# Performance work log

Measured on AMD Instinct MI355X. Metric: run time of the kernel, lower is better.

Reference implementation:

```python
import jax, jax.numpy as jnp
import numpy as np

PI = float(np.pi)


def _layernorm(x, g, b, eps=1e-5):
    mu = jnp.mean(x, axis=-1, keepdims=True)
    var = jnp.var(x, axis=-1, keepdims=True)
    return (x - mu) * jax.lax.rsqrt(var + eps) * g + b


def setup_inputs() -> dict:
    key = jax.random.key(0)
    B, L, D, P = 4, 2048, 256, 32
    ks = jax.random.split(key, 16)

    def lin_w(k, fi, fo):
        return (jax.random.normal(k, (fi, fo), dtype=jnp.float32) / np.sqrt(fi)).astype(jnp.float32)

    inp = {
        'x': jax.random.normal(ks[0], (B, L, D), dtype=jnp.float32),
        'pos_phases': jax.random.normal(ks[1], (L, P), dtype=jnp.float32) * PI,
        'w_mem1v': lin_w(ks[2], D, P), 'b_mem1v': jnp.zeros((P,), jnp.float32),
        'w_mem1o': lin_w(ks[3], P, D), 'b_mem1o': jnp.zeros((D,), jnp.float32),
        'w_off': lin_w(ks[4], D + P, P), 'b_off': jnp.zeros((P,), jnp.float32),
        'w_key': lin_w(ks[5], D, P), 'b_key': jnp.zeros((P,), jnp.float32),
        'w_val': lin_w(ks[6], D, D), 'b_val': jnp.zeros((D,), jnp.float32),
        'w_sk1': lin_w(ks[7], 2 * D, D), 'b_sk1': jnp.zeros((D,), jnp.float32),
        'w_sk2': lin_w(ks[8], D, P), 'b_sk2': jnp.zeros((P,), jnp.float32),
        'w_gate': lin_w(ks[9], D, 1), 'b_gate': jnp.zeros((1,), jnp.float32),
        'ln_g': jnp.ones((D,), jnp.float32), 'ln_b': jnp.zeros((D,), jnp.float32),
        'w_out': lin_w(ks[10], D, D), 'b_out': jnp.zeros((D,), jnp.float32),
    }
    return inp


def reference(x, pos_phases, w_mem1v, b_mem1v, w_mem1o, b_mem1o, w_off, b_off,
              w_key, b_key, w_val, b_val, w_sk1, b_sk1, w_sk2, b_sk2,
              w_gate, b_gate, ln_g, ln_b, w_out, b_out):
    B, L, D = x.shape
    P = pos_phases.shape[-1]

    pos_cos = jnp.cos(pos_phases)  # [L,P]
    pos_sin = jnp.sin(pos_phases)

    # Memory 1: flat [B,L,P] phasor cumulative memory
    v1 = x @ w_mem1v + b_mem1v                       # [B,L,P]
    mem1_cos = jnp.cumsum(pos_cos[None] * v1, axis=1)
    mem1_sin = jnp.cumsum(pos_sin[None] * v1, axis=1)

    offset_input = jnp.concatenate([x, jnp.broadcast_to(pos_phases[None], (B, L, P))], axis=-1)
    offset = jnp.tanh(offset_input @ w_off + b_off) * PI
    oc, os = jnp.cos(offset), jnp.sin(offset)
    query_cos = pos_cos[None] * oc - pos_sin[None] * os
    query_sin = pos_sin[None] * oc + pos_cos[None] * os
    pos_ret = (mem1_cos * query_cos + mem1_sin * query_sin) / np.sqrt(P)
    pos_out = pos_ret @ w_mem1o + b_mem1o            # [B,L,D]

    # Memory 2: full [B,L,P,D] phasor KV cumulative memory
    key_phases = jnp.tanh(x @ w_key + b_key) * PI    # [B,L,P]
    key_cos, key_sin = jnp.cos(key_phases), jnp.sin(key_phases)
    values = x @ w_val + b_val                       # [B,L,D]
    store_gate = jax.nn.sigmoid(x @ w_gate + b_gate) # [B,L,1]

    positions = jnp.arange(1, L + 1, dtype=x.dtype)[None, :, None]
    context_avg = jnp.cumsum(x, axis=1) / positions
    h = jax.nn.gelu(jnp.concatenate([x, context_avg], axis=-1) @ w_sk1 + b_sk1, approximate=False)
    storage_phases = jnp.tanh(h @ w_sk2 + b_sk2) * PI  # [B,L,P]

    gated_v = values * store_gate                    # [B,L,D]
    kv_mem_cos = jnp.cumsum(jnp.cos(storage_phases)[..., None] * gated_v[:, :, None, :], axis=1)  # [B,L,P,D]
    kv_mem_sin = jnp.cumsum(jnp.sin(storage_phases)[..., None] * gated_v[:, :, None, :], axis=1)

    gate_cumsum = jnp.clip(jnp.cumsum(store_gate, axis=1), 1.0, None)  # [B,L,1]
    kv_retrieved = jnp.einsum('blpd,blp->bld', kv_mem_cos, key_cos) + \
                   jnp.einsum('blpd,blp->bld', kv_mem_sin, key_sin)
    kv_retrieved = kv_retrieved / (jnp.sqrt(gate_cumsum) * np.sqrt(P))

    combined = pos_out + kv_retrieved
    return x + _layernorm(combined, ln_g, ln_b) @ w_out + b_out
```

## Files before the change

kernel.cpp:

```cpp
#include <hip/hip_runtime.h>
#include <hip/hip_bf16.h>

constexpr int B_ = 4;
constexpr int L_ = 2048;
constexpr int D_ = 256;
constexpr int P_ = 32;
constexpr int CL = 32;
constexpr int NC = L_ / CL;

#define PI_F 3.14159265358979323846f
#define INV_SQRT_P 0.17677669529663687f

typedef __attribute__((ext_vector_type(8))) short short8_t;
typedef __attribute__((ext_vector_type(4))) float floatx4;

static __device__ inline short f2bf(float f) {
  unsigned int u;
  __builtin_memcpy(&u, &f, 4);
  unsigned int r = (u + 0x7fffu + ((u >> 16) & 1u)) >> 16;
  return (short)r;
}
static __device__ inline float bf2f(short s) {
  unsigned int u = ((unsigned int)(unsigned short)s) << 16;
  float f;
  __builtin_memcpy(&f, &u, 4);
  return f;
}

__global__ void wprep(const float* __restrict__ x, const float* __restrict__ pos,
                      const float* __restrict__ w_val, const float* __restrict__ w_mem1v,
                      const float* __restrict__ w_off, const float* __restrict__ b_off,
                      const float* __restrict__ w_key, const float* __restrict__ w_gate,
                      const float* __restrict__ w_sk1, const float* __restrict__ w_out,
                      const float* __restrict__ w_sk2, const float* __restrict__ w_mem1o,
                      short* __restrict__ WA, short* __restrict__ W1,
                      short* __restrict__ WO, short* __restrict__ W2T,
                      short* __restrict__ W1OT,
                      short* __restrict__ xbf, float* __restrict__ poff,
                      float* __restrict__ ctxsum) {
  int blk = blockIdx.x, tid = threadIdx.x;
  if (blk < 384) {
    int idx = blk * 256 + tid;
    int n = idx >> 8, k = idx & 255;
    float v;
    if (n < 256) v = w_val[k * 256 + n];
    else if (n < 288) v = w_mem1v[k * 32 + (n - 256)];
    else if (n < 320) v = w_off[k * 32 + (n - 288)];
    else if (n < 352) v = w_key[k * 32 + (n - 320)];
    else if (n == 352) v = w_gate[k];
    else v = 0.f;
    WA[idx] = f2bf(v);
  } else if (blk < 896) {
    int idx = (blk - 384) * 256 + tid;
    int n = idx >> 9, k = idx & 511;
    W1[idx] = f2bf(w_sk1[k * 256 + n]);
  } else if (blk < 1152) {
    int idx = (blk - 896) * 256 + tid;
    int n = idx >> 8, k = idx & 255;
    WO[idx] = f2bf(w_out[k * 256 + n]);
  } else if (blk < 1184) {
    int idx = (blk - 1152) * 256 + tid;
    int p = idx >> 8, k = idx & 255;
    W2T[idx] = f2bf(w_sk2[k * 32 + p]);
  } else if (blk < 1216) {
    int idx = (blk - 1184) * 256 + tid;
    int d = idx >> 5, p = idx & 31;
    W1OT[idx] = f2bf(w_mem1o[p * 256 + d]);
  } else if (blk < 3264) {
    int idx = ((blk - 1216) * 256 + tid) * 4;
    float4 v = *(const float4*)&x[idx];
    short4 o;
    o.x = f2bf(v.x); o.y = f2bf(v.y); o.z = f2bf(v.z); o.w = f2bf(v.w);
    *(short4*)&xbf[idx] = o;
  } else if (blk < 3520) {
    int idx = (blk - 3264) * 256 + tid;
    int l = idx >> 5, p = idx & 31;
    float a = b_off[p];
#pragma unroll 8
    for (int j = 0; j < 32; ++j) a += pos[l * 32 + j] * w_off[(256 + j) * 32 + p];
    poff[idx] = a;
  } else {
    int c2 = blk - 3520;
    int b = c2 >> 6, ch = c2 & 63;
    int xb = (b * L_ + ch * 32) * 256 + tid;
    float s = 0.f;
#pragma unroll 8
    for (int i = 0; i < 32; ++i) s += x[xb + i * 256];
    ctxsum[c2 * 256 + tid] = s;
  }
}

template <int KTILES, int MODE>
__global__ __launch_bounds__(256, 4) void gemm32(const short* __restrict__ A0,
                                                 const short* __restrict__ A1,
                                                 const short* __restrict__ W,
                                                 const float* __restrict__ bias,
                                                 const float* __restrict__ xres,
                                                 float* __restrict__ outf,
                                                 short* __restrict__ outb) {
  __shared__ short As[32][136];
  __shared__ short Bs[64][136];
  int tid = threadIdx.x;
  int mg = blockIdx.x >> 2, ng = blockIdx.x & 3;
  int tok0 = mg * 32, n0 = ng * 64;
  int lane = tid & 63, w = tid >> 6;
  int nw = w * 16;
  floatx4 acc[2] = {{0.f, 0.f, 0.f, 0.f}, {0.f, 0.f, 0.f, 0.f}};
  int r2 = tid >> 4, c8 = tid & 15;
  int ml = lane & 15, quad = lane >> 4, kq = quad * 8;
  const int K = KTILES * 128;

  for (int kt = 0; kt < KTILES; ++kt) {
    const short* Asrc;
    int cb;
    if (KTILES == 4) {
      Asrc = (kt < 2) ? A0 : A1;
      cb = (kt & 1) * 128;
    } else {
      Asrc = A0;
      cb = kt * 128;
    }
#pragma unroll
    for (int pass = 0; pass < 2; ++pass) {
      int row = pass * 16 + r2;
      *(short8_t*)&As[row][c8 * 8] =
          *(const short8_t*)&Asrc[(tok0 + row) * 256 + cb + c8 * 8];
    }
#pragma unroll
    for (int pass = 0; pass < 4; ++pass) {
      int row = pass * 16 + r2;
      *(short8_t*)&Bs[row][c8 * 8] =
          *(const short8_t*)&W[(n0 + row) * K + kt * 128 + c8 * 8];
    }
    __syncthreads();
#pragma unroll
    for (int s = 0; s < 4; ++s) {
      short8_t a0 = *(short8_t*)&As[ml][s * 32 + kq];
      short8_t a1 = *(short8_t*)&As[16 + ml][s * 32 + kq];
      short8_t b0 = *(short8_t*)&Bs[nw + ml][s * 32 + kq];
      acc[0] = __builtin_amdgcn_mfma_f32_16x16x32_bf16(a0, b0, acc[0], 0, 0, 0);
      acc[1] = __builtin_amdgcn_mfma_f32_16x16x32_bf16(a1, b0, acc[1], 0, 0, 0);
    }
    __syncthreads();
  }
  int n = n0 + nw + ml;
  float bv = bias ? bias[n] : 0.f;
#pragma unroll
  for (int mt = 0; mt < 2; ++mt) {
#pragma unroll
    for (int rg = 0; rg < 4; ++rg) {
      int tok = tok0 + mt * 16 + quad * 4 + rg;
      float v = acc[mt][rg] + bv;
      if (MODE == 1) {
        float g = 0.5f * v * (1.f + erff(v * 0.70710678118654752f));
        outb[tok * 256 + n] = f2bf(g);
      } else {
        outf[tok * 256 + n] = xres[tok * 256 + n] + v;
      }
    }
  }
}

__global__ __launch_bounds__(384, 3) void gemmA3(const short* __restrict__ xbf,
                                                 const short* __restrict__ WA,
                                                 const float* __restrict__ pos,
                                                 const float* __restrict__ poff,
                                                 const float* __restrict__ b_mem1v,
                                                 const float* __restrict__ b_key,
                                                 const float* __restrict__ b_gate,
                                                 const float* __restrict__ b_val,
                                                 float* __restrict__ m1cT,
                                                 float* __restrict__ m1sT,
                                                 float* __restrict__ qc,
                                                 float* __restrict__ qs,
                                                 short* __restrict__ K2bf,
                                                 short* __restrict__ gvT,
                                                 float* __restrict__ sg) {
  __shared__ float YL[16][132];
  __shared__ float gsh[16];
  int tid = threadIdx.x;
  int lane = tid & 63, w = tid >> 6;
  int ml = lane & 15, quad = lane >> 4, kq = quad * 8;
  int bc = blockIdx.x;
  int bc32 = bc >> 1, half = bc & 1;
  int tok0 = bc * 16;
  floatx4 acc[4] = {};
  const short* A0p = &xbf[(tok0 + ml) * 256 + kq];
  const short* Bp = &WA[(w * 64 + ml) * 256 + kq];
#pragma unroll
  for (int ks = 0; ks < 8; ++ks) {
    short8_t a0 = *(const short8_t*)(A0p + ks * 32);
#pragma unroll
    for (int nt = 0; nt < 4; ++nt) {
      short8_t b = *(const short8_t*)(Bp + nt * 16 * 256 + ks * 32);
      acc[nt] = __builtin_amdgcn_mfma_f32_16x16x32_bf16(a0, b, acc[nt], 0, 0, 0);
    }
  }
  if (w >= 4) {
#pragma unroll
    for (int nt = 0; nt < 4; ++nt) {
      int col = (w - 4) * 64 + nt * 16 + ml;
#pragma unroll
      for (int r = 0; r < 4; ++r)
        YL[quad * 4 + r][col] = acc[nt][r];
    }
  }
  __syncthreads();
  if (tid < 256) {
#pragma unroll
    for (int it = 0; it < 2; ++it) {
      int idx = it * 256 + tid;
      int t = idx >> 5, p = idx & 31;
      int tok = tok0 + t, l = tok & (L_ - 1);
      int b = tok >> 11;
      float v1 = YL[t][p] + b_mem1v[p];
      float ph = pos[l * 32 + p];
      float pc = cosf(ph), ps = sinf(ph);
      int idxT = (b * 32 + p) * L_ + l;
      m1cT[idxT] = pc * v1;
      m1sT[idxT] = ps * v1;
      float off = tanhf(YL[t][32 + p] + poff[l * 32 + p]) * PI_F;
      float oc = cosf(off), os = sinf(off);
      int gidx = tok * 32 + p;
      qc[gidx] = pc * oc - ps * os;
      qs[gidx] = ps * oc + pc * os;
      float kp = tanhf(YL[t][64 + p] + b_key[p]) * PI_F;
      K2bf[tok * 64 + p] = f2bf(cosf(kp));
      K2bf[tok * 64 + 32 + p] = f2bf(sinf(kp));
      if (p == 0) {
        float g = 1.f / (1.f + expf(-(YL[t][96] + b_gate[0])));
        sg[tok] = g;
        gsh[t] = g;
      }
    }
  }
  __syncthreads();
  if (w < 4) {
#pragma unroll
    for (int nt = 0; nt < 4; ++nt) {
      int d = w * 64 + nt * 16 + ml;
      float bv = b_val[d];
      int t0 = quad * 4;
      short4 o;
      o.x = f2bf((acc[nt][0] + bv) * gsh[t0 + 0]);
      o.y = f2bf((acc[nt][1] + bv) * gsh[t0 + 1]);
      o.z = f2bf((acc[nt][2] + bv) * gsh[t0 + 2]);
      o.w = f2bf((acc[nt][3] + bv) * gsh[t0 + 3]);
      *(short4*)&gvT[(bc32 * 256 + d) * 32 + half * 16 + t0] = o;
    }
  }
}

__global__ void scan_all(float* __restrict__ m1cT, float* __restrict__ m1sT,
                         float* __restrict__ sg, const float* __restrict__ x,
                         const float* __restrict__ ctxsum, short* __restrict__ ctxbf) {
  int blk = blockIdx.x;
  int tid = threadIdx.x;
  if (blk >= 260) {
    int c2 = blk - 260;
    int b = c2 >> 6, ch = c2 & 63;
    float run = 0.f;
    int sb = b * 64 * 256 + tid;
    int c = 0;
    for (; c + 8 <= ch; c += 8) {
      float t0 = ctxsum[sb + (c + 0) * 256];
      float t1 = ctxsum[sb + (c + 1) * 256];
      float t2 = ctxsum[sb + (c + 2) * 256];
      float t3 = ctxsum[sb + (c + 3) * 256];
      float t4 = ctxsum[sb + (c + 4) * 256];
      float t5 = ctxsum[sb + (c + 5) * 256];
      float t6 = ctxsum[sb + (c + 6) * 256];
      float t7 = ctxsum[sb + (c + 7) * 256];
      run += ((t0 + t1) + (t2 + t3)) + ((t4 + t5) + (t6 + t7));
    }
    for (; c < ch; ++c) run += ctxsum[sb + c * 256];
    int xb = (b * L_ + ch * 32) * 256 + tid;
#pragma unroll 8
    for (int i = 0; i < 32; ++i) {
      run += x[xb + i * 256];
      int l = ch * 32 + i;
      ctxbf[xb + i * 256] = f2bf(run / (float)(l + 1));
    }
    return;
  }
  int lane = tid & 63, wid = tid >> 6;
  __shared__ float wsum[4];
  float carry = 0.f;
  float* arr;
  int base;
  if (blk < 256) {
    arr = (blk < 128) ? m1cT : m1sT;
    base = (blk & 127) * L_;
  } else {
    arr = sg;
    base = (blk - 256) * L_;
  }
  float v[8];
#pragma unroll
  for (int i = 0; i < 8; ++i) v[i] = arr[base + i * 256 + tid];
#pragma unroll
  for (int i = 0; i < 8; ++i) {
    float vv = v[i];
#pragma unroll
    for (int off = 1; off < 64; off <<= 1) {
      float n = __shfl_up(vv, off, 64);
      if (lane >= off) vv += n;
    }
    if (lane == 63) wsum[wid] = vv;
    __syncthreads();
    float add = carry;
    for (int w = 0; w < wid; ++w) add += wsum[w];
    arr[base + i * 256 + tid] = vv + add;
    carry += wsum[0] + wsum[1] + wsum[2] + wsum[3];
    __syncthreads();
  }
}

__global__ __launch_bounds__(256, 2) void kernelCD(const short* __restrict__ hs,
                                                   const short* __restrict__ W2T,
                                                   const float* __restrict__ b_sk2,
                                                   const short* __restrict__ gvT,
                                                   short* __restrict__ SPbf,
                                                   short* __restrict__ UT) {
  __shared__ __align__(16) short SPL[64][40];
  int tid = threadIdx.x;
  int bc = blockIdx.x >> 1, dh = blockIdx.x & 1;
  int tok0 = bc * 32;
  int lane = tid & 63, w = tid >> 6;
  int ml = lane & 15, quad = lane >> 4, kq = quad * 8;
  int th = w & 1, ph = w >> 1;
  floatx4 pacc = {};
#pragma unroll
  for (int s = 0; s < 8; ++s) {
    short8_t a = *(const short8_t*)&hs[(tok0 + th * 16 + ml) * 256 + s * 32 + kq];
    short8_t b0 = *(const short8_t*)&W2T[(ph * 16 + ml) * 256 + s * 32 + kq];
    pacc = __builtin_amdgcn_mfma_f32_16x16x32_bf16(a, b0, pacc, 0, 0, 0);
  }
  {
    int p = ph * 16 + ml;
    float bs = b_sk2[p];
#pragma unroll
    for (int r = 0; r < 4; ++r) {
      int tl = th * 16 + quad * 4 + r;
      int tok = tok0 + tl;
      float sp = tanhf(pacc[r] + bs) * PI_F;
      short c = f2bf(cosf(sp)), s = f2bf(sinf(sp));
      SPL[p][tl] = c;
      SPL[32 + p][tl] = s;
      if (dh == 0) {
        SPbf[tok * 64 + p] = c;
        SPbf[tok * 64 + 32 + p] = s;
      }
    }
  }
  __syncthreads();
  short8_t a[4];
#pragma unroll
  for (int mt = 0; mt < 4; ++mt) a[mt] = *(short8_t*)&SPL[mt * 16 + ml][kq];
  floatx4 acc[4][2] = {};
#pragma unroll
  for (int nt = 0; nt < 2; ++nt) {
    int d = dh * 128 + w * 32 + nt * 16 + ml;
    short8_t b = *(const short8_t*)&gvT[(bc * 256 + d) * 32 + kq];
#pragma unroll
    for (int mt = 0; mt < 4; ++mt)
      acc[mt][nt] = __builtin_amdgcn_mfma_f32_16x16x32_bf16(a[mt], b, acc[mt][nt], 0, 0, 0);
  }
#pragma unroll
  for (int mt = 0; mt < 4; ++mt)
#pragma unroll
    for (int nt = 0; nt < 2; ++nt) {
      int d = dh * 128 + w * 32 + nt * 16 + ml;
      short4 o;
      o.x = f2bf(acc[mt][nt][0]);
      o.y = f2bf(acc[mt][nt][1]);
      o.z = f2bf(acc[mt][nt][2]);
      o.w = f2bf(acc[mt][nt][3]);
      *(short4*)&UT[(bc * 256 + d) * 64 + mt * 16 + quad * 4] = o;
    }
}

__global__ void kernelE(short* __restrict__ UT) {
  int tid = blockIdx.x * 256 + threadIdx.x;
  int q = tid & 63;
  int d = (tid >> 6) & 255;
  int b = tid >> 14;
  int base = ((b * NC) * 256 + d) * 64 + q;
  const int cs = 256 * 64;
  short v[64];
#pragma unroll
  for (int c = 0; c < 64; ++c) v[c] = UT[base + c * cs];
  float run = 0.f;
#pragma unroll
  for (int c = 0; c < 64; ++c) {
    UT[base + c * cs] = f2bf(run);
    run += bf2f(v[c]);
  }
}

__global__ __launch_bounds__(512, 2) void kernelFG(const short* __restrict__ UT,
                                                   const short* __restrict__ SPbf,
                                                   const short* __restrict__ K2bf,
                                                   const short* __restrict__ gvT,
                                                   const float* __restrict__ sgc,
                                                   const float* __restrict__ m1cT,
                                                   const float* __restrict__ m1sT,
                                                   const float* __restrict__ qc,
                                                   const float* __restrict__ qs,
                                                   const short* __restrict__ W1OT,
                                                   const float* __restrict__ b_mem1o,
                                                   const float* __restrict__ ln_g,
                                                   const float* __restrict__ ln_b,
                                                   short* __restrict__ cbn) {
  __shared__ __align__(16) short SL[32][40];
  __shared__ __align__(16) short PR[32][40];
  __shared__ float CMB[32][260];
  __shared__ float scl[32], mu_s[32], rs_s[32];
  int tid = threadIdx.x;
  int bc = blockIdx.x;
  int lbase = bc * CL;
  int bb = bc >> 6, lloc = (bc & 63) * 32;
  if (tid < 32) scl[tid] = rsqrtf(fmaxf(sgc[lbase + tid], 1.f)) * INV_SQRT_P;
#pragma unroll
  for (int it = 0; it < 2; ++it) {
    int i = it * 512 + tid;
    int p = i >> 5, t = i & 31;
    int gT = (bb * 32 + p) * L_ + lloc + t;
    int g = (lbase + t) * 32 + p;
    PR[t][p] = f2bf((m1cT[gT] * qc[g] + m1sT[gT] * qs[g]) * INV_SQRT_P);
  }
  int lane = tid & 63, w = tid >> 6;
  int ml = lane & 15, quad = lane >> 4, kq = quad * 8;
  int d0 = w * 32;
  floatx4 acc[2][2] = {};
  short8_t ka0 = *(const short8_t*)&K2bf[(lbase + ml) * 64 + kq];
  short8_t ka1 = *(const short8_t*)&K2bf[(lbase + 16 + ml) * 64 + kq];
  short8_t kb0 = *(const short8_t*)&K2bf[(lbase + ml) * 64 + 32 + kq];
  short8_t kb1 = *(const short8_t*)&K2bf[(lbase + 16 + ml) * 64 + 32 + kq];
#pragma unroll
  for (int nt = 0; nt < 2; ++nt) {
    short8_t b = *(const short8_t*)&UT[(bc * 256 + d0 + nt * 16 + ml) * 64 + kq];
    acc[0][nt] = __builtin_amdgcn_mfma_f32_16x16x32_bf16(ka0, b, acc[0][nt], 0, 0, 0);
    acc[1][nt] = __builtin_amdgcn_mfma_f32_16x16x32_bf16(ka1, b, acc[1][nt], 0, 0, 0);
  }
  if (w == 0) {
    floatx4 sacc[2][2] = {};
#pragma unroll
    for (int ks2 = 0; ks2 < 2; ++ks2) {
      short8_t a0 = (ks2 == 0) ? ka0 : kb0;
      short8_t a1 = (ks2 == 0) ? ka1 : kb1;
      short8_t b0 = *(const short8_t*)&SPbf[(lbase + ml) * 64 + ks2 * 32 + kq];
      short8_t b1 = *(const short8_t*)&SPbf[(lbase + 16 + ml) * 64 + ks2 * 32 + kq];
      sacc[0][0] = __builtin_amdgcn_mfma_f32_16x16x32_bf16(a0, b0, sacc[0][0], 0, 0, 0);
      sacc[0][1] = __builtin_amdgcn_mfma_f32_16x16x32_bf16(a0, b1, sacc[0][1], 0, 0, 0);
      sacc[1][0] = __builtin_amdgcn_mfma_f32_16x16x32_bf16(a1, b0, sacc[1][0], 0, 0, 0);
      sacc[1][1] = __builtin_amdgcn_mfma_f32_16x16x32_bf16(a1, b1, sacc[1][1], 0, 0, 0);
    }
#pragma unroll
    for (int mt = 0; mt < 2; ++mt)
#pragma unroll
      for (int nt = 0; nt < 2; ++nt)
#pragma unroll
        for (int r = 0; r < 4; ++r) {
          int trow = mt * 16 + quad * 4 + r;
          int scol = nt * 16 + ml;
          float v = (scol <= trow) ? sacc[mt][nt][r] : 0.f;
          SL[trow][scol] = f2bf(v);
        }
  }
  __syncthreads();
#pragma unroll
  for (int nt = 0; nt < 2; ++nt) {
    short8_t b = *(const short8_t*)&UT[(bc * 256 + d0 + nt * 16 + ml) * 64 + 32 + kq];
    acc[0][nt] = __builtin_amdgcn_mfma_f32_16x16x32_bf16(kb0, b, acc[0][nt], 0, 0, 0);
    acc[1][nt] = __builtin_amdgcn_mfma_f32_16x16x32_bf16(kb1, b, acc[1][nt], 0, 0, 0);
  }
  {
    short8_t a0 = *(short8_t*)&SL[ml][kq];
    short8_t a1 = *(short8_t*)&SL[16 + ml][kq];
#pragma unroll
    for (int nt = 0; nt < 2; ++nt) {
      short8_t b = *(const short8_t*)&gvT[(bc * 256 + d0 + nt * 16 + ml) * 32 + kq];
      acc[0][nt] = __builtin_amdgcn_mfma_f32_16x16x32_bf16(a0, b, acc[0][nt], 0, 0, 0);
      acc[1][nt] = __builtin_amdgcn_mfma_f32_16x16x32_bf16(a1, b, acc[1][nt], 0, 0, 0);
    }
  }
  floatx4 macc[2][2] = {};
  {
    short8_t a0 = *(short8_t*)&PR[ml][kq];
    short8_t a1 = *(short8_t*)&PR[16 + ml][kq];
#pragma unroll
    for (int nt = 0; nt < 2; ++nt) {
      short8_t b = *(const short8_t*)&W1OT[(d0 + nt * 16 + ml) * 32 + kq];
      macc[0][nt] = __builtin_amdgcn_mfma_f32_16x16x32_bf16(a0, b, macc[0][nt], 0, 0, 0);
      macc[1][nt] = __builtin_amdgcn_mfma_f32_16x16x32_bf16(a1, b, macc[1][nt], 0, 0, 0);
    }
  }
#pragma unroll
  for (int mt = 0; mt < 2; ++mt)
#pragma unroll
    for (int nt = 0; nt < 2; ++nt) {
      int d = d0 + nt * 16 + ml;
      float bm = b_mem1o[d];
#pragma unroll
      for (int r = 0; r < 4; ++r) {
        int t = mt * 16 + quad * 4 + r;
        CMB[t][d] = acc[mt][nt][r] * scl[t] + macc[mt][nt][r] + bm;
      }
    }
  __syncthreads();
  {
    int t = tid >> 4, g = tid & 15;
    float s = 0.f, s2 = 0.f;
#pragma unroll
    for (int j = 0; j < 16; ++j) {
      float v = CMB[t][g + j * 16];
      s += v;
      s2 += v * v;
    }
#pragma unroll
    for (int m = 1; m < 16; m <<= 1) {
      s += __shfl_xor(s, m, 64);
      s2 += __shfl_xor(s2, m, 64);
    }
    if (g == 0) {
      float mu = s / (float)D_;
      float var = s2 / (float)D_ - mu * mu;
      mu_s[t] = mu;
      rs_s[t] = rsqrtf(var + 1e-5f);
    }
  }
  __syncthreads();
  {
    int d = tid & 255, th = tid >> 8;
    float lg = ln_g[d], lb = ln_b[d];
#pragma unroll
    for (int i = 0; i < 16; ++i) {
      int t = th * 16 + i;
      cbn[(lbase + t) * 256 + d] = f2bf((CMB[t][d] - mu_s[t]) * rs_s[t] * lg + lb);
    }
  }
}

extern "C" void kernel_launch(void* const* d_in, const int* in_sizes, int n_in,
                              void* d_out, int out_size, void* d_ws, size_t ws_size,
                              hipStream_t stream) {
  const float* x = (const float*)d_in[0];
  const float* pos = (const float*)d_in[1];
  const float* w_mem1v = (const float*)d_in[2];
  const float* b_mem1v = (const float*)d_in[3];
  const float* w_mem1o = (const float*)d_in[4];
  const float* b_mem1o = (const float*)d_in[5];
  const float* w_off = (const float*)d_in[6];
  const float* b_off = (const float*)d_in[7];
  const float* w_key = (const float*)d_in[8];
  const float* b_key = (const float*)d_in[9];
  const float* w_val = (const float*)d_in[10];
  const float* b_val = (const float*)d_in[11];
  const float* w_sk1 = (const float*)d_in[12];
  const float* b_sk1 = (const float*)d_in[13];
  const float* w_sk2 = (const float*)d_in[14];
  const float* b_sk2 = (const float*)d_in[15];
  const float* w_gate = (const float*)d_in[16];
  const float* b_gate = (const float*)d_in[17];
  const float* ln_g = (const float*)d_in[18];
  const float* ln_b = (const float*)d_in[19];
  const float* w_out = (const float*)d_in[20];
  const float* b_out = (const float*)d_in[21];
  float* out = (float*)d_out;
  float* ws = (float*)d_ws;

  const int BLP = B_ * L_ * P_;
  const int BLD = B_ * L_ * D_;
  float* m1cT = ws;
  float* m1sT = m1cT + BLP;
  float* qc = m1sT + BLP;
  float* qs = qc + BLP;
  float* sg = qs + BLP;
  float* poff = sg + B_ * L_;
  float* ctxsum = poff + L_ * P_;
  short* UT = (short*)(ctxsum + B_ * 64 * 256);
  short* xbf = UT + (size_t)B_ * NC * 256 * 64;
  short* cbn = xbf;
  short* ctxbf = xbf + BLD;
  short* hs = ctxbf + BLD;
  short* gvT = hs + BLD;
  short* K2bf = gvT + BLD;
  short* SPbf = K2bf + B_ * L_ * 64;
  short* WA = SPbf + B_ * L_ * 64;
  short* W1 = WA + 384 * 256;
  short* WO = W1 + 256 * 512;
  short* W2T = WO + 256 * 256;
  short* W1OT = W2T + 32 * 256;

  wprep<<<3776, 256, 0, stream>>>(x, pos, w_val, w_mem1v, w_off, b_off, w_key, w_gate,
                                  w_sk1, w_out, w_sk2, w_mem1o, WA, W1, WO, W2T, W1OT,
                                  xbf, poff, ctxsum);
  gemmA3<<<512, 384, 0, stream>>>(xbf, WA, pos, poff, b_mem1v, b_key, b_gate, b_val,
                                  m1cT, m1sT, qc, qs, K2bf, gvT, sg);
  scan_all<<<516, 256, 0, stream>>>(m1cT, m1sT, sg, x, ctxsum, ctxbf);
  gemm32<4, 1><<<256 * 4, 256, 0, stream>>>(xbf, ctxbf, W1, b_sk1, nullptr, nullptr, hs);
  kernelCD<<<512, 256, 0, stream>>>(hs, W2T, b_sk2, gvT, SPbf, UT);
  kernelE<<<256, 256, 0, stream>>>(UT);
  kernelFG<<<B_ * NC, 512, 0, stream>>>(UT, SPbf, K2bf, gvT, sg, m1cT, m1sT, qc, qs,
                                        W1OT, b_mem1o, ln_g, ln_b, cbn);
  gemm32<2, 2><<<256 * 4, 256, 0, stream>>>(cbn, nullptr, WO, b_out, x, out, nullptr);
}
```

Measured before the change: 171.5 us.

## Fuse sk1 GEMM into CD kernel, fuse output GEMM into FG, split chunk scan

The sk1 GELU GEMM now runs inside the storage-phase/UT kernel, so the hs intermediate no longer goes through global memory. The output projection and residual add move into the layernorm kernel, which drops the cbn round trip and one launch. The chunk-prefix scan kernel now uses two threads per column that exchange partial sums through a shuffle, doubling its parallelism. The trade-off is fewer blocks (256) with larger LDS use and weights read directly from global memory without LDS tiling.

```diff
diff --git a/kernel.cpp b/kernel.cpp
--- a/kernel.cpp
+++ b/kernel.cpp
@@ -90,77 +90,6 @@
   }
 }
 
-template <int KTILES, int MODE>
-__global__ __launch_bounds__(256, 4) void gemm32(const short* __restrict__ A0,
-                                                 const short* __restrict__ A1,
-                                                 const short* __restrict__ W,
-                                                 const float* __restrict__ bias,
-                                                 const float* __restrict__ xres,
-                                                 float* __restrict__ outf,
-                                                 short* __restrict__ outb) {
-  __shared__ short As[32][136];
-  __shared__ short Bs[64][136];
-  int tid = threadIdx.x;
-  int mg = blockIdx.x >> 2, ng = blockIdx.x & 3;
-  int tok0 = mg * 32, n0 = ng * 64;
-  int lane = tid & 63, w = tid >> 6;
-  int nw = w * 16;
-  floatx4 acc[2] = {{0.f, 0.f, 0.f, 0.f}, {0.f, 0.f, 0.f, 0.f}};
-  int r2 = tid >> 4, c8 = tid & 15;
-  int ml = lane & 15, quad = lane >> 4, kq = quad * 8;
-  const int K = KTILES * 128;
-
-  for (int kt = 0; kt < KTILES; ++kt) {
-    const short* Asrc;
-    int cb;
-    if (KTILES == 4) {
-      Asrc = (kt < 2) ? A0 : A1;
-      cb = (kt & 1) * 128;
-    } else {
-      Asrc = A0;
-      cb = kt * 128;
-    }
-#pragma unroll
-    for (int pass = 0; pass < 2; ++pass) {
-      int row = pass * 16 + r2;
-      *(short8_t*)&As[row][c8 * 8] =
-          *(const short8_t*)&Asrc[(tok0 + row) * 256 + cb + c8 * 8];
-    }
-#pragma unroll
-    for (int pass = 0; pass < 4; ++pass) {
-      int row = pass * 16 + r2;
-      *(short8_t*)&Bs[row][c8 * 8] =
-          *(const short8_t*)&W[(n0 + row) * K + kt * 128 + c8 * 8];
-    }
-    __syncthreads();
-#pragma unroll
-    for (int s = 0; s < 4; ++s) {
-      short8_t a0 = *(short8_t*)&As[ml][s * 32 + kq];
-      short8_t a1 = *(short8_t*)&As[16 + ml][s * 32 + kq];
-      short8_t b0 = *(short8_t*)&Bs[nw + ml][s * 32 + kq];
-      acc[0] = __builtin_amdgcn_mfma_f32_16x16x32_bf16(a0, b0, acc[0], 0, 0, 0);
-      acc[1] = __builtin_amdgcn_mfma_f32_16x16x32_bf16(a1, b0, acc[1], 0, 0, 0);
-    }
-    __syncthreads();
-  }
-  int n = n0 + nw + ml;
-  float bv = bias ? bias[n] : 0.f;
-#pragma unroll
-  for (int mt = 0; mt < 2; ++mt) {
-#pragma unroll
-    for (int rg = 0; rg < 4; ++rg) {
-      int tok = tok0 + mt * 16 + quad * 4 + rg;
-      float v = acc[mt][rg] + bv;
-      if (MODE == 1) {
-        float g = 0.5f * v * (1.f + erff(v * 0.70710678118654752f));
-        outb[tok * 256 + n] = f2bf(g);
-      } else {
-        outf[tok * 256 + n] = xres[tok * 256 + n] + v;
-      }
-    }
-  }
-}
-
 __global__ __launch_bounds__(384, 3) void gemmA3(const short* __restrict__ xbf,
                                                  const short* __restrict__ WA,
                                                  const float* __restrict__ pos,
@@ -316,27 +245,79 @@
   }
 }
 
-__global__ __launch_bounds__(256, 2) void kernelCD(const short* __restrict__ hs,
-                                                   const short* __restrict__ W2T,
-                                                   const float* __restrict__ b_sk2,
-                                                   const short* __restrict__ gvT,
-                                                   short* __restrict__ SPbf,
-                                                   short* __restrict__ UT) {
-  __shared__ __align__(16) short SPL[64][40];
+union __align__(16) CDMem {
+  short As[32][520];
+  struct { short HS[32][280]; short SPL[64][40]; } h;
+};
+__global__ __launch_bounds__(512, 4) void gemmCD(const short* __restrict__ xbf,
+                                                 const short* __restrict__ ctxbf,
+                                                 const short* __restrict__ W1,
+                                                 const float* __restrict__ b_sk1,
+                                                 const short* __restrict__ W2T,
+                                                 const float* __restrict__ b_sk2,
+                                                 const short* __restrict__ gvT,
+                                                 short* __restrict__ SPbf,
+                                                 short* __restrict__ UT) {
+  __shared__ CDMem sm;
   int tid = threadIdx.x;
-  int bc = blockIdx.x >> 1, dh = blockIdx.x & 1;
+  int bc = blockIdx.x;
   int tok0 = bc * 32;
   int lane = tid & 63, w = tid >> 6;
   int ml = lane & 15, quad = lane >> 4, kq = quad * 8;
-  int th = w & 1, ph = w >> 1;
-  floatx4 pacc = {};
-#pragma unroll
-  for (int s = 0; s < 8; ++s) {
-    short8_t a = *(const short8_t*)&hs[(tok0 + th * 16 + ml) * 256 + s * 32 + kq];
-    short8_t b0 = *(const short8_t*)&W2T[(ph * 16 + ml) * 256 + s * 32 + kq];
-    pacc = __builtin_amdgcn_mfma_f32_16x16x32_bf16(a, b0, pacc, 0, 0, 0);
-  }
-  {
+#pragma unroll
+  for (int pass = 0; pass < 4; ++pass) {
+    int idx = pass * 512 + tid;
+    int row = idx >> 6, c8 = idx & 63;
+    int col = c8 * 8;
+    const short* src = (col < 256) ? &xbf[(tok0 + row) * 256 + col]
+                                   : &ctxbf[(tok0 + row) * 256 + col - 256];
+    *(short8_t*)&sm.As[row][col] = *(const short8_t*)src;
+  }
+  __syncthreads();
+  int n0w = w * 32;
+  floatx4 acc[2][2] = {};
+#pragma unroll
+  for (int kt = 0; kt < 16; ++kt) {
+    short8_t a0 = *(short8_t*)&sm.As[ml][kt * 32 + kq];
+    short8_t a1 = *(short8_t*)&sm.As[16 + ml][kt * 32 + kq];
+    short8_t b0 = *(const short8_t*)&W1[(n0w + ml) * 512 + kt * 32 + kq];
+    short8_t b1 = *(const short8_t*)&W1[(n0w + 16 + ml) * 512 + kt * 32 + kq];
+    acc[0][0] = __builtin_amdgcn_mfma_f32_16x16x32_bf16(a0, b0, acc[0][0], 0, 0, 0);
+    acc[0][1] = __builtin_amdgcn_mfma_f32_16x16x32_bf16(a0, b1, acc[0][1], 0, 0, 0);
+    acc[1][0] = __builtin_amdgcn_mfma_f32_16x16x32_bf16(a1, b0, acc[1][0], 0, 0, 0);
+    acc[1][1] = __builtin_amdgcn_mfma_f32_16x16x32_bf16(a1, b1, acc[1][1], 0, 0, 0);
+  }
+  short hv[2][2][4];
+#pragma unroll
+  for (int nt = 0; nt < 2; ++nt) {
+    float bv = b_sk1[n0w + nt * 16 + ml];
+#pragma unroll
+    for (int mt = 0; mt < 2; ++mt)
+#pragma unroll
+      for (int r = 0; r < 4; ++r) {
+        float v = acc[mt][nt][r] + bv;
+        float g = 0.5f * v * (1.f + erff(v * 0.70710678118654752f));
+        hv[mt][nt][r] = f2bf(g);
+      }
+  }
+  __syncthreads();
+#pragma unroll
+  for (int mt = 0; mt < 2; ++mt)
+#pragma unroll
+    for (int nt = 0; nt < 2; ++nt)
+#pragma unroll
+      for (int r = 0; r < 4; ++r)
+        sm.h.HS[mt * 16 + quad * 4 + r][n0w + nt * 16 + ml] = hv[mt][nt][r];
+  __syncthreads();
+  if (w < 4) {
+    int th = w & 1, ph = w >> 1;
+    floatx4 pacc = {};
+#pragma unroll
+    for (int s = 0; s < 8; ++s) {
+      short8_t a = *(short8_t*)&sm.h.HS[th * 16 + ml][s * 32 + kq];
+      short8_t b0 = *(const short8_t*)&W2T[(ph * 16 + ml) * 256 + s * 32 + kq];
+      pacc = __builtin_amdgcn_mfma_f32_16x16x32_bf16(a, b0, pacc, 0, 0, 0);
+    }
     int p = ph * 16 + ml;
     float bs = b_sk2[p];
 #pragma unroll
@@ -344,92 +325,108 @@
       int tl = th * 16 + quad * 4 + r;
       int tok = tok0 + tl;
       float sp = tanhf(pacc[r] + bs) * PI_F;
-      short c = f2bf(cosf(sp)), s = f2bf(sinf(sp));
-      SPL[p][tl] = c;
-      SPL[32 + p][tl] = s;
-      if (dh == 0) {
-        SPbf[tok * 64 + p] = c;
-        SPbf[tok * 64 + 32 + p] = s;
-      }
+      short c = f2bf(cosf(sp)), s2 = f2bf(sinf(sp));
+      sm.h.SPL[p][tl] = c;
+      sm.h.SPL[32 + p][tl] = s2;
+      SPbf[tok * 64 + p] = c;
+      SPbf[tok * 64 + 32 + p] = s2;
     }
   }
   __syncthreads();
   short8_t a[4];
 #pragma unroll
-  for (int mt = 0; mt < 4; ++mt) a[mt] = *(short8_t*)&SPL[mt * 16 + ml][kq];
-  floatx4 acc[4][2] = {};
+  for (int mt = 0; mt < 4; ++mt) a[mt] = *(short8_t*)&sm.h.SPL[mt * 16 + ml][kq];
+  floatx4 acc3[4][2] = {};
 #pragma unroll
   for (int nt = 0; nt < 2; ++nt) {
-    int d = dh * 128 + w * 32 + nt * 16 + ml;
+    int d = w * 32 + nt * 16 + ml;
     short8_t b = *(const short8_t*)&gvT[(bc * 256 + d) * 32 + kq];
 #pragma unroll
     for (int mt = 0; mt < 4; ++mt)
-      acc[mt][nt] = __builtin_amdgcn_mfma_f32_16x16x32_bf16(a[mt], b, acc[mt][nt], 0, 0, 0);
+      acc3[mt][nt] = __builtin_amdgcn_mfma_f32_16x16x32_bf16(a[mt], b, acc3[mt][nt], 0, 0, 0);
   }
 #pragma unroll
   for (int mt = 0; mt < 4; ++mt)
 #pragma unroll
     for (int nt = 0; nt < 2; ++nt) {
-      int d = dh * 128 + w * 32 + nt * 16 + ml;
+      int d = w * 32 + nt * 16 + ml;
       short4 o;
-      o.x = f2bf(acc[mt][nt][0]);
-      o.y = f2bf(acc[mt][nt][1]);
-      o.z = f2bf(acc[mt][nt][2]);
-      o.w = f2bf(acc[mt][nt][3]);
+      o.x = f2bf(acc3[mt][nt][0]);
+      o.y = f2bf(acc3[mt][nt][1]);
+      o.z = f2bf(acc3[mt][nt][2]);
+      o.w = f2bf(acc3[mt][nt][3]);
       *(short4*)&UT[(bc * 256 + d) * 64 + mt * 16 + quad * 4] = o;
     }
 }
 
 __global__ void kernelE(short* __restrict__ UT) {
-  int tid = blockIdx.x * 256 + threadIdx.x;
-  int q = tid & 63;
-  int d = (tid >> 6) & 255;
-  int b = tid >> 14;
-  int base = ((b * NC) * 256 + d) * 64 + q;
+  int t = blockIdx.x * 256 + threadIdx.x;
+  int pi = t >> 1, half = t & 1;
+  int q = pi & 63;
+  int d = (pi >> 6) & 255;
+  int b = pi >> 14;
   const int cs = 256 * 64;
-  short v[64];
-#pragma unroll
-  for (int c = 0; c < 64; ++c) v[c] = UT[base + c * cs];
-  float run = 0.f;
-#pragma unroll
-  for (int c = 0; c < 64; ++c) {
+  int base = ((b * NC) * 256 + d) * 64 + q + half * 32 * cs;
+  short v[32];
+#pragma unroll
+  for (int c = 0; c < 32; ++c) v[c] = UT[base + c * cs];
+  float tot = 0.f;
+#pragma unroll
+  for (int c = 0; c < 32; ++c) tot += bf2f(v[c]);
+  float other = __shfl_xor(tot, 1, 64);
+  float run = half ? other : 0.f;
+#pragma unroll
+  for (int c = 0; c < 32; ++c) {
     UT[base + c * cs] = f2bf(run);
     run += bf2f(v[c]);
   }
 }
 
-__global__ __launch_bounds__(512, 2) void kernelFG(const short* __restrict__ UT,
-                                                   const short* __restrict__ SPbf,
-                                                   const short* __restrict__ K2bf,
-                                                   const short* __restrict__ gvT,
-                                                   const float* __restrict__ sgc,
-                                                   const float* __restrict__ m1cT,
-                                                   const float* __restrict__ m1sT,
-                                                   const float* __restrict__ qc,
-                                                   const float* __restrict__ qs,
-                                                   const short* __restrict__ W1OT,
-                                                   const float* __restrict__ b_mem1o,
-                                                   const float* __restrict__ ln_g,
-                                                   const float* __restrict__ ln_b,
-                                                   short* __restrict__ cbn) {
-  __shared__ __align__(16) short SL[32][40];
-  __shared__ __align__(16) short PR[32][40];
-  __shared__ float CMB[32][260];
-  __shared__ float scl[32], mu_s[32], rs_s[32];
-  int tid = threadIdx.x;
+struct __align__(16) FGMem {
+  short SL[32][40];
+  short PR[32][40];
+  float CMB[32][260];
+  short CBN[32][280];
+  float LG[256], LB[256];
+  float scl[32], mu_s[32], rs_s[32];
+};
+__global__ __launch_bounds__(512, 4) void fgOut(const short* __restrict__ UT,
+                                                const short* __restrict__ SPbf,
+                                                const short* __restrict__ K2bf,
+                                                const short* __restrict__ gvT,
+                                                const float* __restrict__ sgc,
+                                                const float* __restrict__ m1cT,
+                                                const float* __restrict__ m1sT,
+                                                const float* __restrict__ qc,
+                                                const float* __restrict__ qs,
+                                                const short* __restrict__ W1OT,
+                                                const float* __restrict__ b_mem1o,
+                                                const float* __restrict__ ln_g,
+                                                const float* __restrict__ ln_b,
+                                                const short* __restrict__ WO,
+                                                const float* __restrict__ b_out,
+                                                const float* __restrict__ x,
+                                                float* __restrict__ out) {
+  __shared__ FGMem sm;
+  int tid5 = threadIdx.x;
   int bc = blockIdx.x;
   int lbase = bc * CL;
   int bb = bc >> 6, lloc = (bc & 63) * 32;
-  if (tid < 32) scl[tid] = rsqrtf(fmaxf(sgc[lbase + tid], 1.f)) * INV_SQRT_P;
+  if (tid5 < 32) sm.scl[tid5] = rsqrtf(fmaxf(sgc[lbase + tid5], 1.f)) * INV_SQRT_P;
+  if (tid5 >= 256 && tid5 < 512) {
+    int d = tid5 - 256;
+    sm.LG[d] = ln_g[d];
+    sm.LB[d] = ln_b[d];
+  }
 #pragma unroll
   for (int it = 0; it < 2; ++it) {
-    int i = it * 512 + tid;
-    int p = i >> 5, t = i & 31;
-    int gT = (bb * 32 + p) * L_ + lloc + t;
-    int g = (lbase + t) * 32 + p;
-    PR[t][p] = f2bf((m1cT[gT] * qc[g] + m1sT[gT] * qs[g]) * INV_SQRT_P);
-  }
-  int lane = tid & 63, w = tid >> 6;
+    int i = it * 512 + tid5;
+    int pp = i >> 5, t = i & 31;
+    int gT = (bb * 32 + pp) * L_ + lloc + t;
+    int g = (lbase + t) * 32 + pp;
+    sm.PR[t][pp] = f2bf((m1cT[gT] * qc[g] + m1sT[gT] * qs[g]) * INV_SQRT_P);
+  }
+  int lane = tid5 & 63, w = tid5 >> 6;
   int ml = lane & 15, quad = lane >> 4, kq = quad * 8;
   int d0 = w * 32;
   floatx4 acc[2][2] = {};
@@ -465,7 +462,7 @@
           int trow = mt * 16 + quad * 4 + r;
           int scol = nt * 16 + ml;
           float v = (scol <= trow) ? sacc[mt][nt][r] : 0.f;
-          SL[trow][scol] = f2bf(v);
+          sm.SL[trow][scol] = f2bf(v);
         }
   }
   __syncthreads();
@@ -476,8 +473,8 @@
     acc[1][nt] = __builtin_amdgcn_mfma_f32_16x16x32_bf16(kb1, b, acc[1][nt], 0, 0, 0);
   }
   {
-    short8_t a0 = *(short8_t*)&SL[ml][kq];
-    short8_t a1 = *(short8_t*)&SL[16 + ml][kq];
+    short8_t a0 = *(short8_t*)&sm.SL[ml][kq];
+    short8_t a1 = *(short8_t*)&sm.SL[16 + ml][kq];
 #pragma unroll
     for (int nt = 0; nt < 2; ++nt) {
       short8_t b = *(const short8_t*)&gvT[(bc * 256 + d0 + nt * 16 + ml) * 32 + kq];
@@ -487,8 +484,8 @@
   }
   floatx4 macc[2][2] = {};
   {
-    short8_t a0 = *(short8_t*)&PR[ml][kq];
-    short8_t a1 = *(short8_t*)&PR[16 + ml][kq];
+    short8_t a0 = *(short8_t*)&sm.PR[ml][kq];
+    short8_t a1 = *(short8_t*)&sm.PR[16 + ml][kq];
 #pragma unroll
     for (int nt = 0; nt < 2; ++nt) {
       short8_t b = *(const short8_t*)&W1OT[(d0 + nt * 16 + ml) * 32 + kq];
@@ -505,16 +502,16 @@
 #pragma unroll
       for (int r = 0; r < 4; ++r) {
         int t = mt * 16 + quad * 4 + r;
-        CMB[t][d] = acc[mt][nt][r] * scl[t] + macc[mt][nt][r] + bm;
+        sm.CMB[t][d] = acc[mt][nt][r] * sm.scl[t] + macc[mt][nt][r] + bm;
       }
     }
   __syncthreads();
   {
-    int t = tid >> 4, g = tid & 15;
+    int t = tid5 >> 4, g = tid5 & 15;
     float s = 0.f, s2 = 0.f;
 #pragma unroll
     for (int j = 0; j < 16; ++j) {
-      float v = CMB[t][g + j * 16];
+      float v = sm.CMB[t][g + j * 16];
       s += v;
       s2 += v * v;
     }
@@ -526,19 +523,41 @@
     if (g == 0) {
       float mu = s / (float)D_;
       float var = s2 / (float)D_ - mu * mu;
-      mu_s[t] = mu;
-      rs_s[t] = rsqrtf(var + 1e-5f);
-    }
-  }
-  __syncthreads();
-  {
-    int d = tid & 255, th = tid >> 8;
-    float lg = ln_g[d], lb = ln_b[d];
-#pragma unroll
-    for (int i = 0; i < 16; ++i) {
-      int t = th * 16 + i;
-      cbn[(lbase + t) * 256 + d] = f2bf((CMB[t][d] - mu_s[t]) * rs_s[t] * lg + lb);
-    }
+      sm.mu_s[t] = mu;
+      sm.rs_s[t] = rsqrtf(var + 1e-5f);
+    }
+  }
+  __syncthreads();
+#pragma unroll
+  for (int it = 0; it < 16; ++it) {
+    int i = it * 512 + tid5;
+    int t = i >> 8, d = i & 255;
+    sm.CBN[t][d] = f2bf((sm.CMB[t][d] - sm.mu_s[t]) * sm.rs_s[t] * sm.LG[d] + sm.LB[d]);
+  }
+  __syncthreads();
+  floatx4 acc2[2][2] = {};
+#pragma unroll
+  for (int kt = 0; kt < 8; ++kt) {
+    short8_t a0 = *(short8_t*)&sm.CBN[ml][kt * 32 + kq];
+    short8_t a1 = *(short8_t*)&sm.CBN[16 + ml][kt * 32 + kq];
+#pragma unroll
+    for (int nt = 0; nt < 2; ++nt) {
+      short8_t b = *(const short8_t*)&WO[(d0 + nt * 16 + ml) * 256 + kt * 32 + kq];
+      acc2[0][nt] = __builtin_amdgcn_mfma_f32_16x16x32_bf16(a0, b, acc2[0][nt], 0, 0, 0);
+      acc2[1][nt] = __builtin_amdgcn_mfma_f32_16x16x32_bf16(a1, b, acc2[1][nt], 0, 0, 0);
+    }
+  }
+#pragma unroll
+  for (int nt = 0; nt < 2; ++nt) {
+    int n = d0 + nt * 16 + ml;
+    float bv = b_out[n];
+#pragma unroll
+    for (int mt = 0; mt < 2; ++mt)
+#pragma unroll
+      for (int r = 0; r < 4; ++r) {
+        int tok = lbase + mt * 16 + quad * 4 + r;
+        out[tok * 256 + n] = x[tok * 256 + n] + acc2[mt][nt][r] + bv;
+      }
   }
 }
 
@@ -581,7 +600,6 @@
   float* ctxsum = poff + L_ * P_;
   short* UT = (short*)(ctxsum + B_ * 64 * 256);
   short* xbf = UT + (size_t)B_ * NC * 256 * 64;
-  short* cbn = xbf;
   short* ctxbf = xbf + BLD;
   short* hs = ctxbf + BLD;
   short* gvT = hs + BLD;
@@ -599,10 +617,8 @@
   gemmA3<<<512, 384, 0, stream>>>(xbf, WA, pos, poff, b_mem1v, b_key, b_gate, b_val,
                                   m1cT, m1sT, qc, qs, K2bf, gvT, sg);
   scan_all<<<516, 256, 0, stream>>>(m1cT, m1sT, sg, x, ctxsum, ctxbf);
-  gemm32<4, 1><<<256 * 4, 256, 0, stream>>>(xbf, ctxbf, W1, b_sk1, nullptr, nullptr, hs);
-  kernelCD<<<512, 256, 0, stream>>>(hs, W2T, b_sk2, gvT, SPbf, UT);
-  kernelE<<<256, 256, 0, stream>>>(UT);
-  kernelFG<<<B_ * NC, 512, 0, stream>>>(UT, SPbf, K2bf, gvT, sg, m1cT, m1sT, qc, qs,
-                                        W1OT, b_mem1o, ln_g, ln_b, cbn);
-  gemm32<2, 2><<<256 * 4, 256, 0, stream>>>(cbn, nullptr, WO, b_out, x, out, nullptr);
-}
+  gemmCD<<<256, 512, 0, stream>>>(xbf, ctxbf, W1, b_sk1, W2T, b_sk2, gvT, SPbf, UT);
+  kernelE<<<512, 256, 0, stream>>>(UT);
+  fgOut<<<256, 512, 0, stream>>>(UT, SPbf, K2bf, gvT, sg, m1cT, m1sT, qc, qs,
+                                 W1OT, b_mem1o, ln_g, ln_b, WO, b_out, x, out);
+}
```

Result: no change. 172.3 us (+0.5%).
